# Kernel optimization log

Hardware: AMD Instinct MI355X
Metric: run time of the kernel (lower is better)

## Reference

```python
import jax, jax.numpy as jnp
import numpy as np

T, B = 2048, 32
LIS, SPE, ATT = 1024, 1024, 512


def setup_inputs() -> dict:
    key = jax.random.key(0)
    ks = jax.random.split(key, 10)
    s = 0.02
    return {
        "listener_state": jax.random.normal(ks[0], (T, B, LIS), jnp.float32),
        "speller_state": jax.random.normal(ks[1], (B, SPE), jnp.float32),
        "listener_len": jax.random.randint(ks[2], (B,), 1, T + 1),
        "batch_size": B,
        "W_score": jax.random.normal(ks[3], (LIS, ATT), jnp.float32) * s,
        "b_score": jnp.zeros((ATT,), jnp.float32),
        "W_value": jax.random.normal(ks[4], (LIS, ATT), jnp.float32) * s,
        "b_value": jnp.zeros((ATT,), jnp.float32),
        "W_proj": jax.random.normal(ks[5], (SPE, ATT), jnp.float32) * s,
        "b_proj": jnp.zeros((ATT,), jnp.float32),
    }


def reference(listener_state, speller_state, listener_len, batch_size,
              W_score, b_score, W_value, b_value, W_proj, b_proj):
    # batch_first=False path: [T,B,D] -> [B,T,D]
    x = jnp.transpose(listener_state, (1, 0, 2))
    keys = jax.nn.relu(x @ W_score + b_score)          # [B,T,A]
    vals = jax.nn.relu(x @ W_value + b_value)          # [B,T,A]
    query = jax.nn.relu(speller_state @ W_proj + b_proj)  # [B,A]
    scores = jnp.einsum('ba,bta->bt', query, keys)     # [B,T]
    # vectorized length mask: additive -100 past valid length (faithful to source)
    t = jnp.arange(keys.shape[1])
    mask = jnp.where(t[None, :] >= listener_len[:, None], -100.0, 0.0)
    attn = jax.nn.softmax(scores + mask, axis=1)       # [B,T]
    context = jnp.einsum('bt,bta->ba', attn, vals)     # [B,A]
    return (context, attn)
```

## Files before the change

kernel.cpp:

```cpp
#include <hip/hip_runtime.h>
#include <hip/hip_bf16.h>
#include <hip/hip_fp16.h>

#define T_DIM 2048
#define B_DIM 32
#define LIS_DIM 1024
#define SPE_DIM 1024
#define ATT_DIM 512

typedef _Float16 f16x8 __attribute__((ext_vector_type(8)));
typedef _Float16 f16x4 __attribute__((ext_vector_type(4)));
typedef float f32x4 __attribute__((ext_vector_type(4)));

__global__ void transpose_w_kernel(const float* __restrict__ Ws,
                                   const float* __restrict__ Wv,
                                   _Float16* __restrict__ WTf) {
  __shared__ float t17[1024 * 17];
  int blk = blockIdx.x;
  int mat = blk >> 5, ct = blk & 31;
  int tid = threadIdx.x;
  const float* W = mat ? Wv : Ws;
  for (int e = tid; e < 16384; e += 256) {
    int k = e >> 4, c = e & 15;
    t17[k * 17 + c] = W[(size_t)k * ATT_DIM + ct * 16 + c];
  }
  __syncthreads();
  int wv4 = tid >> 6, lane = tid & 63, lo = lane & 15, hi = lane >> 4;
  for (int ks = wv4; ks < 32; ks += 4) {
    f16x8 h;
#pragma unroll
    for (int j = 0; j < 8; ++j)
      h[j] = (_Float16)t17[(ks * 32 + hi * 8 + j) * 17 + lo];
    ((f16x8*)WTf)[((size_t)((mat * 32 + ct) * 32 + ks)) * 64 + lane] = h;
  }
}

__global__ void query_kernel(const float* __restrict__ spe,
                             const float* __restrict__ Wp,
                             const float* __restrict__ bp,
                             float* __restrict__ q) {
  __shared__ float s[SPE_DIM];
  int b = blockIdx.x;
  for (int i = threadIdx.x; i < SPE_DIM; i += 256) s[i] = spe[(size_t)b * SPE_DIM + i];
  __syncthreads();
  for (int a = threadIdx.x; a < ATT_DIM; a += 256) {
    float acc = bp[a];
    for (int l = 0; l < SPE_DIM; ++l)
      acc = fmaf(s[l], Wp[(size_t)l * ATT_DIM + a], acc);
    q[(size_t)b * ATT_DIM + a] = fmaxf(acc, 0.f);
  }
}

__global__ __launch_bounds__(512, 2)
void dual_gemm_kernel(const float* __restrict__ x,
                      const _Float16* __restrict__ WTf,
                      const float* __restrict__ bs,
                      const float* __restrict__ bv,
                      const float* __restrict__ q,
                      float* __restrict__ scores,
                      _Float16* __restrict__ vals_p) {
  __shared__ __align__(16) char A_lds[2][16384];
  __shared__ float bk_s[ATT_DIM], bv_s[ATT_DIM], q_s[ATT_DIM];
  __shared__ float red_s[64];

  const int tid = threadIdx.x;
  const int blk = blockIdx.x;
  const int b = blk & 31;
  const int tc = blk >> 5;
  const int t0 = tc * 64;

  bk_s[tid] = bs[tid];
  bv_s[tid] = bv[tid];
  q_s[tid] = q[(size_t)b * ATT_DIM + tid];
  if (tid < 64) red_s[tid] = 0.f;

  const float* xb = x + (size_t)b * LIS_DIM;
  const int wv = tid >> 6;
  const int lane = tid & 63;
  const int lo = lane & 15;
  const int hi = lane >> 4;

  f32x4 sl[4];
  auto stage_load = [&](int c) {
    const int k0 = c * 128;
#pragma unroll
    for (int it = 0; it < 4; ++it) {
      int idx = it * 512 + tid;
      int row = idx >> 5;
      int c4 = idx & 31;
      sl[it] = __builtin_nontemporal_load(
          (const f32x4*)(xb + (size_t)(t0 + row) * (B_DIM * LIS_DIM) + k0) + c4);
    }
  };
  auto stage_write = [&](int c) {
    char* buf = A_lds[c & 1];
#pragma unroll
    for (int it = 0; it < 4; ++it) {
      int idx = it * 512 + tid;
      int row = idx >> 5;
      int c4 = idx & 31;
      f16x4 h;
      h[0] = (_Float16)sl[it][0]; h[1] = (_Float16)sl[it][1];
      h[2] = (_Float16)sl[it][2]; h[3] = (_Float16)sl[it][3];
      int off = (row * 256 + c4 * 8) ^ ((row & 7) << 4);
      *(f16x4*)(buf + off) = h;
    }
  };

  f32x4 kacc[4][4], vacc[4][4];
#pragma unroll
  for (int m = 0; m < 4; ++m)
#pragma unroll
    for (int n = 0; n < 4; ++n) {
      kacc[m][n] = (f32x4){0.f, 0.f, 0.f, 0.f};
      vacc[m][n] = (f32x4){0.f, 0.f, 0.f, 0.f};
    }

  stage_load(0);
  stage_write(0);
  __syncthreads();

  const f16x8* Wf = (const f16x8*)WTf;
  f16x8 wkf[2][4], wvf[2][4];
#pragma unroll
  for (int n = 0; n < 4; ++n) {
    wkf[0][n] = Wf[(size_t)((wv * 4 + n) * 32 + 0) * 64 + lane];
    wvf[0][n] = Wf[(size_t)((32 + wv * 4 + n) * 32 + 0) * 64 + lane];
  }

  for (int c = 0; c < 8; ++c) {
    if (c < 7) stage_load(c + 1);
    const char* buf = A_lds[c & 1];
#pragma unroll
    for (int kki = 0; kki < 4; ++kki) {
      const int ks = c * 4 + kki;
      const int kp = (ks + 1 < 32) ? ks + 1 : 31;
      const int cur = kki & 1, nxt = cur ^ 1;
#pragma unroll
      for (int n = 0; n < 4; ++n) {
        wkf[nxt][n] = Wf[(size_t)((wv * 4 + n) * 32 + kp) * 64 + lane];
        wvf[nxt][n] = Wf[(size_t)((32 + wv * 4 + n) * 32 + kp) * 64 + lane];
      }
      f16x8 bx[4];
#pragma unroll
      for (int m = 0; m < 4; ++m) {
        int row = m * 16 + lo;
        int off = (row * 256 + kki * 64 + hi * 16) ^ ((row & 7) << 4);
        bx[m] = *(const f16x8*)(buf + off);
      }
#pragma unroll
      for (int n = 0; n < 4; ++n)
#pragma unroll
        for (int m = 0; m < 4; ++m) {
          kacc[m][n] = __builtin_amdgcn_mfma_f32_16x16x32_f16(wkf[cur][n], bx[m], kacc[m][n], 0, 0, 0);
          vacc[m][n] = __builtin_amdgcn_mfma_f32_16x16x32_f16(wvf[cur][n], bx[m], vacc[m][n], 0, 0, 0);
        }
    }
    if (c < 7) stage_write(c + 1);
    __syncthreads();
  }

  _Float16* vp = vals_p + ((size_t)(b * 32 + tc) * 8 + wv) * 4096;
#pragma unroll
  for (int m = 0; m < 4; ++m)
#pragma unroll
    for (int n = 0; n < 4; ++n) {
      int col = wv * 64 + n * 16 + hi * 4;
      f16x4 h;
#pragma unroll
      for (int r = 0; r < 4; ++r)
        h[r] = (_Float16)fmaxf(vacc[m][n][r] + bv_s[col + r], 0.f);
      __builtin_nontemporal_store(h, (f16x4*)(vp + (m * 4 + n) * 256 + lane * 4));
    }

  float sr[4] = {0.f, 0.f, 0.f, 0.f};
#pragma unroll
  for (int m = 0; m < 4; ++m)
#pragma unroll
    for (int n = 0; n < 4; ++n) {
      int col = wv * 64 + n * 16 + hi * 4;
#pragma unroll
      for (int r = 0; r < 4; ++r)
        sr[m] += q_s[col + r] * fmaxf(kacc[m][n][r] + bk_s[col + r], 0.f);
    }
#pragma unroll
  for (int m = 0; m < 4; ++m) {
    sr[m] += __shfl_xor(sr[m], 16, 64);
    sr[m] += __shfl_xor(sr[m], 32, 64);
    if (lane < 16) atomicAdd(&red_s[m * 16 + lo], sr[m]);
  }
  __syncthreads();
  if (tid < 64) scores[(size_t)b * T_DIM + t0 + tid] = red_s[tid];
}

__global__ void softmax_kernel(const float* __restrict__ scores,
                               const int* __restrict__ llen,
                               float* __restrict__ attn_out,
                               float* __restrict__ ctx_out) {
  __shared__ float rmax[4], rsum[4];
  int b = blockIdx.x, tid = threadIdx.x;
  int L = llen[b];
  float v[8];
  float mx = -1e30f;
  for (int i = 0; i < 8; ++i) {
    int t = i * 256 + tid;
    float s = scores[(size_t)b * T_DIM + t];
    if (t >= L) s -= 100.f;
    v[i] = s;
    mx = fmaxf(mx, s);
  }
  for (int d = 1; d < 64; d <<= 1) mx = fmaxf(mx, __shfl_xor(mx, d, 64));
  if ((tid & 63) == 0) rmax[tid >> 6] = mx;
  __syncthreads();
  mx = fmaxf(fmaxf(rmax[0], rmax[1]), fmaxf(rmax[2], rmax[3]));
  float sum = 0.f;
  for (int i = 0; i < 8; ++i) { v[i] = expf(v[i] - mx); sum += v[i]; }
  for (int d = 1; d < 64; d <<= 1) sum += __shfl_xor(sum, d, 64);
  if ((tid & 63) == 0) rsum[tid >> 6] = sum;
  __syncthreads();
  sum = rsum[0] + rsum[1] + rsum[2] + rsum[3];
  float inv = 1.f / sum;
  for (int i = 0; i < 8; ++i) {
    int t = i * 256 + tid;
    attn_out[(size_t)b * T_DIM + t] = v[i] * inv;
  }
  for (int i = tid; i < ATT_DIM; i += 256) ctx_out[(size_t)b * ATT_DIM + i] = 0.f;
}

__global__ __launch_bounds__(512)
void ctx_kernel(const _Float16* __restrict__ vals_p,
                const float* __restrict__ attn,
                float* __restrict__ ctx) {
  __shared__ float attn_s[256];
  int blk = blockIdx.x;
  int b = blk >> 3, tcg = blk & 7;
  int tid = threadIdx.x;
  int wv = tid >> 6, lane = tid & 63, lo = lane & 15, hi = lane >> 4;
  if (tid < 256) attn_s[tid] = attn[(size_t)b * T_DIM + tcg * 256 + tid];
  __syncthreads();
  float cacc[4][4] = {};
  for (int i = 0; i < 4; ++i) {
    int tc = tcg * 4 + i;
    const _Float16* vp = vals_p + ((size_t)(b * 32 + tc) * 8 + wv) * 4096;
#pragma unroll
    for (int m = 0; m < 4; ++m) {
      float w = attn_s[i * 64 + m * 16 + lo];
#pragma unroll
      for (int n = 0; n < 4; ++n) {
        f16x4 v = __builtin_nontemporal_load(
            (const f16x4*)(vp + (m * 4 + n) * 256 + lane * 4));
#pragma unroll
        for (int r = 0; r < 4; ++r) cacc[n][r] += w * (float)v[r];
      }
    }
  }
#pragma unroll
  for (int n = 0; n < 4; ++n)
#pragma unroll
    for (int r = 0; r < 4; ++r) {
      float v = cacc[n][r];
      v += __shfl_xor(v, 1, 64);
      v += __shfl_xor(v, 2, 64);
      v += __shfl_xor(v, 4, 64);
      v += __shfl_xor(v, 8, 64);
      if (lo == 0)
        atomicAdd(&ctx[(size_t)b * ATT_DIM + wv * 64 + n * 16 + hi * 4 + r], v);
    }
}

extern "C" void kernel_launch(void* const* d_in, const int* in_sizes, int n_in,
                              void* d_out, int out_size, void* d_ws, size_t ws_size,
                              hipStream_t stream) {
  const float* x   = (const float*)d_in[0];
  const float* spe = (const float*)d_in[1];
  const int*   len = (const int*)d_in[2];
  const float* Ws  = (const float*)d_in[4];
  const float* bs  = (const float*)d_in[5];
  const float* Wv  = (const float*)d_in[6];
  const float* bv  = (const float*)d_in[7];
  const float* Wp  = (const float*)d_in[8];
  const float* bp  = (const float*)d_in[9];
  float* out = (float*)d_out;

  char* ws = (char*)d_ws;
  _Float16* WTf  = (_Float16*)ws;
  float* q       = (float*)(ws + (2u << 20));
  float* scores  = (float*)(ws + (2u << 20) + (64u << 10));
  _Float16* vals = (_Float16*)(ws + (4u << 20));

  transpose_w_kernel<<<dim3(64), dim3(256), 0, stream>>>(Ws, Wv, WTf);
  query_kernel<<<dim3(32), dim3(256), 0, stream>>>(spe, Wp, bp, q);
  dual_gemm_kernel<<<dim3(1024), dim3(512), 0, stream>>>(x, WTf, bs, bv, q, scores, vals);
  softmax_kernel<<<dim3(32), dim3(256), 0, stream>>>(scores, len, out + 16384, out);
  ctx_kernel<<<dim3(256), dim3(512), 0, stream>>>(vals, out + 16384, out);
}
```

Before: 253.9 us.

## Fuse softmax-weighted context into dual GEMM with flash-style partial reductions

Each dual GEMM block now applies the length mask, computes a local max and exp-sum over its 64 timesteps, and reduces exp-weighted ReLU values into a per-block partial context vector. This removes the fp16 vals intermediate (written and then re-read through global memory) and replaces the separate softmax and context kernels with one small final kernel. That kernel rescales the partials by exp(local max minus global max) and also writes the attention weights. The cost is extra epilogue work and shuffle reductions in the GEMM kernel, plus a small fp32 partial buffer.

New measurement: 257.9 us. About the same (+1.6%).

```diff
diff --git a/kernel.cpp b/kernel.cpp
--- a/kernel.cpp
+++ b/kernel.cpp
@@ -57,17 +57,22 @@
                       const float* __restrict__ bs,
                       const float* __restrict__ bv,
                       const float* __restrict__ q,
+                      const int* __restrict__ llen,
                       float* __restrict__ scores,
-                      _Float16* __restrict__ vals_p) {
+                      float* __restrict__ partM,
+                      float* __restrict__ partZ,
+                      float* __restrict__ Npart) {
   __shared__ __align__(16) char A_lds[2][16384];
   __shared__ float bk_s[ATT_DIM], bv_s[ATT_DIM], q_s[ATT_DIM];
   __shared__ float red_s[64];
+  __shared__ float pb_s[64];
 
   const int tid = threadIdx.x;
   const int blk = blockIdx.x;
   const int b = blk & 31;
   const int tc = blk >> 5;
   const int t0 = tc * 64;
+  const int L = llen[b];
 
   bk_s[tid] = bs[tid];
   bv_s[tid] = bv[tid];
@@ -160,19 +165,6 @@
     __syncthreads();
   }
 
-  _Float16* vp = vals_p + ((size_t)(b * 32 + tc) * 8 + wv) * 4096;
-#pragma unroll
-  for (int m = 0; m < 4; ++m)
-#pragma unroll
-    for (int n = 0; n < 4; ++n) {
-      int col = wv * 64 + n * 16 + hi * 4;
-      f16x4 h;
-#pragma unroll
-      for (int r = 0; r < 4; ++r)
-        h[r] = (_Float16)fmaxf(vacc[m][n][r] + bv_s[col + r], 0.f);
-      __builtin_nontemporal_store(h, (f16x4*)(vp + (m * 4 + n) * 256 + lane * 4));
-    }
-
   float sr[4] = {0.f, 0.f, 0.f, 0.f};
 #pragma unroll
   for (int m = 0; m < 4; ++m)
@@ -190,82 +182,92 @@
     if (lane < 16) atomicAdd(&red_s[m * 16 + lo], sr[m]);
   }
   __syncthreads();
-  if (tid < 64) scores[(size_t)b * T_DIM + t0 + tid] = red_s[tid];
-}
-
-__global__ void softmax_kernel(const float* __restrict__ scores,
-                               const int* __restrict__ llen,
-                               float* __restrict__ attn_out,
-                               float* __restrict__ ctx_out) {
-  __shared__ float rmax[4], rsum[4];
+
+  if (wv == 0) {
+    float s = red_s[lane] + ((t0 + lane) >= L ? -100.f : 0.f);
+    scores[(size_t)b * T_DIM + t0 + lane] = s;
+    float mx = s;
+#pragma unroll
+    for (int d = 1; d < 64; d <<= 1) mx = fmaxf(mx, __shfl_xor(mx, d, 64));
+    float p = expf(s - mx);
+    float z = p;
+#pragma unroll
+    for (int d = 1; d < 64; d <<= 1) z += __shfl_xor(z, d, 64);
+    pb_s[lane] = p;
+    if (lane == 0) {
+      partM[b * 32 + tc] = mx;
+      partZ[b * 32 + tc] = z;
+    }
+  }
+  __syncthreads();
+
+  float cs[4][4] = {};
+#pragma unroll
+  for (int m = 0; m < 4; ++m) {
+    float p = pb_s[m * 16 + lo];
+#pragma unroll
+    for (int n = 0; n < 4; ++n) {
+      int col = wv * 64 + n * 16 + hi * 4;
+#pragma unroll
+      for (int r = 0; r < 4; ++r)
+        cs[n][r] += p * fmaxf(vacc[m][n][r] + bv_s[col + r], 0.f);
+    }
+  }
+#pragma unroll
+  for (int n = 0; n < 4; ++n)
+#pragma unroll
+    for (int r = 0; r < 4; ++r) {
+      cs[n][r] += __shfl_xor(cs[n][r], 1, 64);
+      cs[n][r] += __shfl_xor(cs[n][r], 2, 64);
+      cs[n][r] += __shfl_xor(cs[n][r], 4, 64);
+      cs[n][r] += __shfl_xor(cs[n][r], 8, 64);
+    }
+  if (lo == 0) {
+    float* Np = Npart + ((size_t)(b * 32 + tc)) * ATT_DIM;
+#pragma unroll
+    for (int n = 0; n < 4; ++n) {
+      f32x4 v = {cs[n][0], cs[n][1], cs[n][2], cs[n][3]};
+      *(f32x4*)(Np + wv * 64 + n * 16 + hi * 4) = v;
+    }
+  }
+}
+
+__global__ __launch_bounds__(512)
+void final_kernel(const float* __restrict__ scores,
+                  const float* __restrict__ partM,
+                  const float* __restrict__ partZ,
+                  const float* __restrict__ Npart,
+                  float* __restrict__ ctx_out,
+                  float* __restrict__ attn_out) {
+  __shared__ float sc_s[32];
+  __shared__ float MZ[2];
   int b = blockIdx.x, tid = threadIdx.x;
-  int L = llen[b];
-  float v[8];
-  float mx = -1e30f;
-  for (int i = 0; i < 8; ++i) {
-    int t = i * 256 + tid;
-    float s = scores[(size_t)b * T_DIM + t];
-    if (t >= L) s -= 100.f;
-    v[i] = s;
-    mx = fmaxf(mx, s);
-  }
-  for (int d = 1; d < 64; d <<= 1) mx = fmaxf(mx, __shfl_xor(mx, d, 64));
-  if ((tid & 63) == 0) rmax[tid >> 6] = mx;
-  __syncthreads();
-  mx = fmaxf(fmaxf(rmax[0], rmax[1]), fmaxf(rmax[2], rmax[3]));
-  float sum = 0.f;
-  for (int i = 0; i < 8; ++i) { v[i] = expf(v[i] - mx); sum += v[i]; }
-  for (int d = 1; d < 64; d <<= 1) sum += __shfl_xor(sum, d, 64);
-  if ((tid & 63) == 0) rsum[tid >> 6] = sum;
-  __syncthreads();
-  sum = rsum[0] + rsum[1] + rsum[2] + rsum[3];
-  float inv = 1.f / sum;
-  for (int i = 0; i < 8; ++i) {
-    int t = i * 256 + tid;
-    attn_out[(size_t)b * T_DIM + t] = v[i] * inv;
-  }
-  for (int i = tid; i < ATT_DIM; i += 256) ctx_out[(size_t)b * ATT_DIM + i] = 0.f;
-}
-
-__global__ __launch_bounds__(512)
-void ctx_kernel(const _Float16* __restrict__ vals_p,
-                const float* __restrict__ attn,
-                float* __restrict__ ctx) {
-  __shared__ float attn_s[256];
-  int blk = blockIdx.x;
-  int b = blk >> 3, tcg = blk & 7;
-  int tid = threadIdx.x;
-  int wv = tid >> 6, lane = tid & 63, lo = lane & 15, hi = lane >> 4;
-  if (tid < 256) attn_s[tid] = attn[(size_t)b * T_DIM + tcg * 256 + tid];
-  __syncthreads();
-  float cacc[4][4] = {};
+  int lane = tid & 63;
+  if (tid < 64) {
+    float pm = (lane < 32) ? partM[b * 32 + lane] : -1e30f;
+    float mx = pm;
+#pragma unroll
+    for (int d = 1; d < 64; d <<= 1) mx = fmaxf(mx, __shfl_xor(mx, d, 64));
+    float e = (lane < 32) ? expf(pm - mx) : 0.f;
+    float z = ((lane < 32) ? partZ[b * 32 + lane] : 0.f) * e;
+#pragma unroll
+    for (int d = 1; d < 64; d <<= 1) z += __shfl_xor(z, d, 64);
+    if (lane < 32) sc_s[lane] = e;
+    if (lane == 0) { MZ[0] = mx; MZ[1] = 1.f / z; }
+  }
+  __syncthreads();
+  const float M = MZ[0], invZ = MZ[1];
+#pragma unroll
   for (int i = 0; i < 4; ++i) {
-    int tc = tcg * 4 + i;
-    const _Float16* vp = vals_p + ((size_t)(b * 32 + tc) * 8 + wv) * 4096;
-#pragma unroll
-    for (int m = 0; m < 4; ++m) {
-      float w = attn_s[i * 64 + m * 16 + lo];
-#pragma unroll
-      for (int n = 0; n < 4; ++n) {
-        f16x4 v = __builtin_nontemporal_load(
-            (const f16x4*)(vp + (m * 4 + n) * 256 + lane * 4));
-#pragma unroll
-        for (int r = 0; r < 4; ++r) cacc[n][r] += w * (float)v[r];
-      }
-    }
-  }
-#pragma unroll
-  for (int n = 0; n < 4; ++n)
-#pragma unroll
-    for (int r = 0; r < 4; ++r) {
-      float v = cacc[n][r];
-      v += __shfl_xor(v, 1, 64);
-      v += __shfl_xor(v, 2, 64);
-      v += __shfl_xor(v, 4, 64);
-      v += __shfl_xor(v, 8, 64);
-      if (lo == 0)
-        atomicAdd(&ctx[(size_t)b * ATT_DIM + wv * 64 + n * 16 + hi * 4 + r], v);
-    }
+    int t = i * 512 + tid;
+    attn_out[(size_t)b * T_DIM + t] = expf(scores[(size_t)b * T_DIM + t] - M) * invZ;
+  }
+  float acc = 0.f;
+  const float* Np = Npart + (size_t)b * 32 * ATT_DIM;
+#pragma unroll 8
+  for (int tcc = 0; tcc < 32; ++tcc)
+    acc = fmaf(sc_s[tcc], Np[tcc * ATT_DIM + tid], acc);
+  ctx_out[(size_t)b * ATT_DIM + tid] = acc * invZ;
 }
 
 extern "C" void kernel_launch(void* const* d_in, const int* in_sizes, int n_in,
@@ -283,14 +285,17 @@
   float* out = (float*)d_out;
 
   char* ws = (char*)d_ws;
-  _Float16* WTf  = (_Float16*)ws;
-  float* q       = (float*)(ws + (2u << 20));
-  float* scores  = (float*)(ws + (2u << 20) + (64u << 10));
-  _Float16* vals = (_Float16*)(ws + (4u << 20));
+  _Float16* WTf = (_Float16*)ws;
+  float* q      = (float*)(ws + (2u << 20));
+  float* scores = (float*)(ws + (2u << 20) + (64u << 10));
+  float* partM  = (float*)(ws + (2u << 20) + (320u << 10));
+  float* partZ  = (float*)(ws + (2u << 20) + (324u << 10));
+  float* Npart  = (float*)(ws + (2u << 20) + (328u << 10));
 
   transpose_w_kernel<<<dim3(64), dim3(256), 0, stream>>>(Ws, Wv, WTf);
   query_kernel<<<dim3(32), dim3(256), 0, stream>>>(spe, Wp, bp, q);
-  dual_gemm_kernel<<<dim3(1024), dim3(512), 0, stream>>>(x, WTf, bs, bv, q, scores, vals);
-  softmax_kernel<<<dim3(32), dim3(256), 0, stream>>>(scores, len, out + 16384, out);
-  ctx_kernel<<<dim3(256), dim3(512), 0, stream>>>(vals, out + 16384, out);
-}
+  dual_gemm_kernel<<<dim3(1024), dim3(512), 0, stream>>>(
+      x, WTf, bs, bv, q, len, scores, partM, partZ, Npart);
+  final_kernel<<<dim3(32), dim3(512), 0, stream>>>(
+      scores, partM, partZ, Npart, out, out + 16384);
+}
```

## Split dual GEMM by weight matrix with 128-row tiles; merge prep kernels

Applied to the files above, without the earlier changes.

Each GEMM block now computes only one of the key or value projections over a 128-row time tile instead of both over 64 rows, and the block count stays the same. The aim is to halve the per-block weight fragment loads and the accumulator register pressure per matrix. The cost is that every x tile is now read and converted twice, once for keys and once for values. The weight transpose and the query projection are merged into one launch to save a kernel launch, and the vals layout and ctx kernel indexing are updated to the 128-row tiles.

After: 341.7 us. 34.6% more time.

```diff
diff --git a/kernel.cpp b/kernel.cpp
--- a/kernel.cpp
+++ b/kernel.cpp
@@ -12,67 +12,68 @@
 typedef _Float16 f16x4 __attribute__((ext_vector_type(4)));
 typedef float f32x4 __attribute__((ext_vector_type(4)));
 
-__global__ void transpose_w_kernel(const float* __restrict__ Ws,
-                                   const float* __restrict__ Wv,
-                                   _Float16* __restrict__ WTf) {
-  __shared__ float t17[1024 * 17];
+__global__ void prep_kernel(const float* __restrict__ Ws,
+                            const float* __restrict__ Wv,
+                            _Float16* __restrict__ WTf,
+                            const float* __restrict__ spe,
+                            const float* __restrict__ Wp,
+                            const float* __restrict__ bp,
+                            float* __restrict__ q) {
   int blk = blockIdx.x;
-  int mat = blk >> 5, ct = blk & 31;
   int tid = threadIdx.x;
-  const float* W = mat ? Wv : Ws;
-  for (int e = tid; e < 16384; e += 256) {
-    int k = e >> 4, c = e & 15;
-    t17[k * 17 + c] = W[(size_t)k * ATT_DIM + ct * 16 + c];
-  }
-  __syncthreads();
-  int wv4 = tid >> 6, lane = tid & 63, lo = lane & 15, hi = lane >> 4;
-  for (int ks = wv4; ks < 32; ks += 4) {
-    f16x8 h;
-#pragma unroll
-    for (int j = 0; j < 8; ++j)
-      h[j] = (_Float16)t17[(ks * 32 + hi * 8 + j) * 17 + lo];
-    ((f16x8*)WTf)[((size_t)((mat * 32 + ct) * 32 + ks)) * 64 + lane] = h;
-  }
-}
-
-__global__ void query_kernel(const float* __restrict__ spe,
-                             const float* __restrict__ Wp,
-                             const float* __restrict__ bp,
-                             float* __restrict__ q) {
-  __shared__ float s[SPE_DIM];
-  int b = blockIdx.x;
-  for (int i = threadIdx.x; i < SPE_DIM; i += 256) s[i] = spe[(size_t)b * SPE_DIM + i];
-  __syncthreads();
-  for (int a = threadIdx.x; a < ATT_DIM; a += 256) {
-    float acc = bp[a];
-    for (int l = 0; l < SPE_DIM; ++l)
-      acc = fmaf(s[l], Wp[(size_t)l * ATT_DIM + a], acc);
-    q[(size_t)b * ATT_DIM + a] = fmaxf(acc, 0.f);
+  if (blk < 64) {
+    __shared__ float t17[1024 * 17];
+    int mat = blk >> 5, ct = blk & 31;
+    const float* W = mat ? Wv : Ws;
+    for (int e = tid; e < 16384; e += 256) {
+      int k = e >> 4, c = e & 15;
+      t17[k * 17 + c] = W[(size_t)k * ATT_DIM + ct * 16 + c];
+    }
+    __syncthreads();
+    int wv4 = tid >> 6, lane = tid & 63, lo = lane & 15, hi = lane >> 4;
+    for (int ks = wv4; ks < 32; ks += 4) {
+      f16x8 h;
+#pragma unroll
+      for (int j = 0; j < 8; ++j)
+        h[j] = (_Float16)t17[(ks * 32 + hi * 8 + j) * 17 + lo];
+      ((f16x8*)WTf)[((size_t)((mat * 32 + ct) * 32 + ks)) * 64 + lane] = h;
+    }
+  } else {
+    __shared__ float s[SPE_DIM];
+    int b = blk - 64;
+    for (int i = tid; i < SPE_DIM; i += 256) s[i] = spe[(size_t)b * SPE_DIM + i];
+    __syncthreads();
+    for (int a = tid; a < ATT_DIM; a += 256) {
+      float acc = bp[a];
+      for (int l = 0; l < SPE_DIM; ++l)
+        acc = fmaf(s[l], Wp[(size_t)l * ATT_DIM + a], acc);
+      q[(size_t)b * ATT_DIM + a] = fmaxf(acc, 0.f);
+    }
   }
 }
 
 __global__ __launch_bounds__(512, 2)
-void dual_gemm_kernel(const float* __restrict__ x,
-                      const _Float16* __restrict__ WTf,
-                      const float* __restrict__ bs,
-                      const float* __restrict__ bv,
-                      const float* __restrict__ q,
-                      float* __restrict__ scores,
-                      _Float16* __restrict__ vals_p) {
-  __shared__ __align__(16) char A_lds[2][16384];
-  __shared__ float bk_s[ATT_DIM], bv_s[ATT_DIM], q_s[ATT_DIM];
-  __shared__ float red_s[64];
+void gemm_split_kernel(const float* __restrict__ x,
+                       const _Float16* __restrict__ WTf,
+                       const float* __restrict__ bs,
+                       const float* __restrict__ bv,
+                       const float* __restrict__ q,
+                       float* __restrict__ scores,
+                       _Float16* __restrict__ vals_p) {
+  __shared__ __align__(16) char A_lds[2][32768];
+  __shared__ float bias_s[ATT_DIM], q_s[ATT_DIM];
+  __shared__ float red_s[128];
 
   const int tid = threadIdx.x;
   const int blk = blockIdx.x;
-  const int b = blk & 31;
-  const int tc = blk >> 5;
-  const int t0 = tc * 64;
-
-  bk_s[tid] = bs[tid];
-  bv_s[tid] = bv[tid];
+  const int mat = blk & 1;
+  const int b   = (blk >> 1) & 31;
+  const int tc  = blk >> 6;
+  const int t0  = tc * 128;
+
+  bias_s[tid] = mat ? bv[tid] : bs[tid];
   q_s[tid] = q[(size_t)b * ATT_DIM + tid];
-  if (tid < 64) red_s[tid] = 0.f;
+  if (tid < 128) red_s[tid] = 0.f;
 
   const float* xb = x + (size_t)b * LIS_DIM;
   const int wv = tid >> 6;
@@ -80,11 +81,11 @@
   const int lo = lane & 15;
   const int hi = lane >> 4;
 
-  f32x4 sl[4];
+  f32x4 sl[8];
   auto stage_load = [&](int c) {
     const int k0 = c * 128;
 #pragma unroll
-    for (int it = 0; it < 4; ++it) {
+    for (int it = 0; it < 8; ++it) {
       int idx = it * 512 + tid;
       int row = idx >> 5;
       int c4 = idx & 31;
@@ -95,7 +96,7 @@
   auto stage_write = [&](int c) {
     char* buf = A_lds[c & 1];
 #pragma unroll
-    for (int it = 0; it < 4; ++it) {
+    for (int it = 0; it < 8; ++it) {
       int idx = it * 512 + tid;
       int row = idx >> 5;
       int c4 = idx & 31;
@@ -107,26 +108,22 @@
     }
   };
 
-  f32x4 kacc[4][4], vacc[4][4];
-#pragma unroll
-  for (int m = 0; m < 4; ++m)
-#pragma unroll
-    for (int n = 0; n < 4; ++n) {
-      kacc[m][n] = (f32x4){0.f, 0.f, 0.f, 0.f};
-      vacc[m][n] = (f32x4){0.f, 0.f, 0.f, 0.f};
-    }
+  f32x4 acc[8][4];
+#pragma unroll
+  for (int m = 0; m < 8; ++m)
+#pragma unroll
+    for (int n = 0; n < 4; ++n)
+      acc[m][n] = (f32x4){0.f, 0.f, 0.f, 0.f};
 
   stage_load(0);
   stage_write(0);
   __syncthreads();
 
   const f16x8* Wf = (const f16x8*)WTf;
-  f16x8 wkf[2][4], wvf[2][4];
-#pragma unroll
-  for (int n = 0; n < 4; ++n) {
-    wkf[0][n] = Wf[(size_t)((wv * 4 + n) * 32 + 0) * 64 + lane];
-    wvf[0][n] = Wf[(size_t)((32 + wv * 4 + n) * 32 + 0) * 64 + lane];
-  }
+  f16x8 wf[2][4];
+#pragma unroll
+  for (int n = 0; n < 4; ++n)
+    wf[0][n] = Wf[(size_t)((mat * 32 + wv * 4 + n) * 32 + 0) * 64 + lane];
 
   for (int c = 0; c < 8; ++c) {
     if (c < 7) stage_load(c + 1);
@@ -137,13 +134,11 @@
       const int kp = (ks + 1 < 32) ? ks + 1 : 31;
       const int cur = kki & 1, nxt = cur ^ 1;
 #pragma unroll
-      for (int n = 0; n < 4; ++n) {
-        wkf[nxt][n] = Wf[(size_t)((wv * 4 + n) * 32 + kp) * 64 + lane];
-        wvf[nxt][n] = Wf[(size_t)((32 + wv * 4 + n) * 32 + kp) * 64 + lane];
-      }
-      f16x8 bx[4];
-#pragma unroll
-      for (int m = 0; m < 4; ++m) {
+      for (int n = 0; n < 4; ++n)
+        wf[nxt][n] = Wf[(size_t)((mat * 32 + wv * 4 + n) * 32 + kp) * 64 + lane];
+      f16x8 bx[8];
+#pragma unroll
+      for (int m = 0; m < 8; ++m) {
         int row = m * 16 + lo;
         int off = (row * 256 + kki * 64 + hi * 16) ^ ((row & 7) << 4);
         bx[m] = *(const f16x8*)(buf + off);
@@ -151,46 +146,48 @@
 #pragma unroll
       for (int n = 0; n < 4; ++n)
 #pragma unroll
-        for (int m = 0; m < 4; ++m) {
-          kacc[m][n] = __builtin_amdgcn_mfma_f32_16x16x32_f16(wkf[cur][n], bx[m], kacc[m][n], 0, 0, 0);
-          vacc[m][n] = __builtin_amdgcn_mfma_f32_16x16x32_f16(wvf[cur][n], bx[m], vacc[m][n], 0, 0, 0);
-        }
+        for (int m = 0; m < 8; ++m)
+          acc[m][n] = __builtin_amdgcn_mfma_f32_16x16x32_f16(wf[cur][n], bx[m], acc[m][n], 0, 0, 0);
     }
     if (c < 7) stage_write(c + 1);
     __syncthreads();
   }
 
-  _Float16* vp = vals_p + ((size_t)(b * 32 + tc) * 8 + wv) * 4096;
-#pragma unroll
-  for (int m = 0; m < 4; ++m)
-#pragma unroll
-    for (int n = 0; n < 4; ++n) {
-      int col = wv * 64 + n * 16 + hi * 4;
-      f16x4 h;
-#pragma unroll
-      for (int r = 0; r < 4; ++r)
-        h[r] = (_Float16)fmaxf(vacc[m][n][r] + bv_s[col + r], 0.f);
-      __builtin_nontemporal_store(h, (f16x4*)(vp + (m * 4 + n) * 256 + lane * 4));
-    }
-
-  float sr[4] = {0.f, 0.f, 0.f, 0.f};
-#pragma unroll
-  for (int m = 0; m < 4; ++m)
-#pragma unroll
-    for (int n = 0; n < 4; ++n) {
-      int col = wv * 64 + n * 16 + hi * 4;
-#pragma unroll
-      for (int r = 0; r < 4; ++r)
-        sr[m] += q_s[col + r] * fmaxf(kacc[m][n][r] + bk_s[col + r], 0.f);
-    }
-#pragma unroll
-  for (int m = 0; m < 4; ++m) {
-    sr[m] += __shfl_xor(sr[m], 16, 64);
-    sr[m] += __shfl_xor(sr[m], 32, 64);
-    if (lane < 16) atomicAdd(&red_s[m * 16 + lo], sr[m]);
-  }
-  __syncthreads();
-  if (tid < 64) scores[(size_t)b * T_DIM + t0 + tid] = red_s[tid];
+  if (mat == 0) {
+    float sr[8];
+#pragma unroll
+    for (int m = 0; m < 8; ++m) sr[m] = 0.f;
+#pragma unroll
+    for (int m = 0; m < 8; ++m)
+#pragma unroll
+      for (int n = 0; n < 4; ++n) {
+        int col = wv * 64 + n * 16 + hi * 4;
+#pragma unroll
+        for (int r = 0; r < 4; ++r)
+          sr[m] += q_s[col + r] * fmaxf(acc[m][n][r] + bias_s[col + r], 0.f);
+      }
+#pragma unroll
+    for (int m = 0; m < 8; ++m) {
+      sr[m] += __shfl_xor(sr[m], 16, 64);
+      sr[m] += __shfl_xor(sr[m], 32, 64);
+      if (lane < 16) atomicAdd(&red_s[m * 16 + lo], sr[m]);
+    }
+    __syncthreads();
+    if (tid < 128) scores[(size_t)b * T_DIM + t0 + tid] = red_s[tid];
+  } else {
+    _Float16* vp = vals_p + ((size_t)(b * 16 + tc) * 8 + wv) * 8192;
+#pragma unroll
+    for (int m = 0; m < 8; ++m)
+#pragma unroll
+      for (int n = 0; n < 4; ++n) {
+        int col = wv * 64 + n * 16 + hi * 4;
+        f16x4 h;
+#pragma unroll
+        for (int r = 0; r < 4; ++r)
+          h[r] = (_Float16)fmaxf(acc[m][n][r] + bias_s[col + r], 0.f);
+        __builtin_nontemporal_store(h, (f16x4*)(vp + (m * 4 + n) * 256 + lane * 4));
+      }
+  }
 }
 
 __global__ void softmax_kernel(const float* __restrict__ scores,
@@ -233,18 +230,18 @@
                 float* __restrict__ ctx) {
   __shared__ float attn_s[256];
   int blk = blockIdx.x;
-  int b = blk >> 3, tcg = blk & 7;
+  int b = blk >> 3, tg = blk & 7;
   int tid = threadIdx.x;
   int wv = tid >> 6, lane = tid & 63, lo = lane & 15, hi = lane >> 4;
-  if (tid < 256) attn_s[tid] = attn[(size_t)b * T_DIM + tcg * 256 + tid];
+  if (tid < 256) attn_s[tid] = attn[(size_t)b * T_DIM + tg * 256 + tid];
   __syncthreads();
   float cacc[4][4] = {};
-  for (int i = 0; i < 4; ++i) {
-    int tc = tcg * 4 + i;
-    const _Float16* vp = vals_p + ((size_t)(b * 32 + tc) * 8 + wv) * 4096;
-#pragma unroll
-    for (int m = 0; m < 4; ++m) {
-      float w = attn_s[i * 64 + m * 16 + lo];
+  for (int i = 0; i < 2; ++i) {
+    int tc = tg * 2 + i;
+    const _Float16* vp = vals_p + ((size_t)(b * 16 + tc) * 8 + wv) * 8192;
+#pragma unroll
+    for (int m = 0; m < 8; ++m) {
+      float w = attn_s[i * 128 + m * 16 + lo];
 #pragma unroll
       for (int n = 0; n < 4; ++n) {
         f16x4 v = __builtin_nontemporal_load(
@@ -288,9 +285,9 @@
   float* scores  = (float*)(ws + (2u << 20) + (64u << 10));
   _Float16* vals = (_Float16*)(ws + (4u << 20));
 
-  transpose_w_kernel<<<dim3(64), dim3(256), 0, stream>>>(Ws, Wv, WTf);
-  query_kernel<<<dim3(32), dim3(256), 0, stream>>>(spe, Wp, bp, q);
-  dual_gemm_kernel<<<dim3(1024), dim3(512), 0, stream>>>(x, WTf, bs, bv, q, scores, vals);
+  prep_kernel<<<dim3(96), dim3(256), 0, stream>>>(Ws, Wv, WTf, spe, Wp, bp, q);
+  gemm_split_kernel<<<dim3(1024), dim3(512), 0, stream>>>(
+      x, WTf, bs, bv, q, scores, vals);
   softmax_kernel<<<dim3(32), dim3(256), 0, stream>>>(scores, len, out + 16384, out);
   ctx_kernel<<<dim3(256), dim3(512), 0, stream>>>(vals, out + 16384, out);
 }
```

## Interleave global prefetch with MFMA steps and merge prep kernels

Applied to the files above, without the earlier changes.

Spreads the next-chunk global loads across the four k-substeps, one slice per substep, instead of issuing them all at once. Each MFMA block is wrapped with explicit barriers, an lgkmcnt wait, a sched_barrier and setprio raised around the MFMAs, so waves stay in lockstep and give priority to matrix work. It also fuses the weight-transpose and query kernels into one launch to save launch overhead. The extra per-substep barriers can add synchronisation stalls.

New measurement: 365.4 us. +43.9%, slower.

```diff
diff --git a/kernel.cpp b/kernel.cpp
--- a/kernel.cpp
+++ b/kernel.cpp
@@ -12,42 +12,43 @@
 typedef _Float16 f16x4 __attribute__((ext_vector_type(4)));
 typedef float f32x4 __attribute__((ext_vector_type(4)));
 
-__global__ void transpose_w_kernel(const float* __restrict__ Ws,
-                                   const float* __restrict__ Wv,
-                                   _Float16* __restrict__ WTf) {
-  __shared__ float t17[1024 * 17];
+__global__ void prep_kernel(const float* __restrict__ Ws,
+                            const float* __restrict__ Wv,
+                            _Float16* __restrict__ WTf,
+                            const float* __restrict__ spe,
+                            const float* __restrict__ Wp,
+                            const float* __restrict__ bp,
+                            float* __restrict__ q) {
   int blk = blockIdx.x;
-  int mat = blk >> 5, ct = blk & 31;
   int tid = threadIdx.x;
-  const float* W = mat ? Wv : Ws;
-  for (int e = tid; e < 16384; e += 256) {
-    int k = e >> 4, c = e & 15;
-    t17[k * 17 + c] = W[(size_t)k * ATT_DIM + ct * 16 + c];
-  }
-  __syncthreads();
-  int wv4 = tid >> 6, lane = tid & 63, lo = lane & 15, hi = lane >> 4;
-  for (int ks = wv4; ks < 32; ks += 4) {
-    f16x8 h;
-#pragma unroll
-    for (int j = 0; j < 8; ++j)
-      h[j] = (_Float16)t17[(ks * 32 + hi * 8 + j) * 17 + lo];
-    ((f16x8*)WTf)[((size_t)((mat * 32 + ct) * 32 + ks)) * 64 + lane] = h;
-  }
-}
-
-__global__ void query_kernel(const float* __restrict__ spe,
-                             const float* __restrict__ Wp,
-                             const float* __restrict__ bp,
-                             float* __restrict__ q) {
-  __shared__ float s[SPE_DIM];
-  int b = blockIdx.x;
-  for (int i = threadIdx.x; i < SPE_DIM; i += 256) s[i] = spe[(size_t)b * SPE_DIM + i];
-  __syncthreads();
-  for (int a = threadIdx.x; a < ATT_DIM; a += 256) {
-    float acc = bp[a];
-    for (int l = 0; l < SPE_DIM; ++l)
-      acc = fmaf(s[l], Wp[(size_t)l * ATT_DIM + a], acc);
-    q[(size_t)b * ATT_DIM + a] = fmaxf(acc, 0.f);
+  if (blk < 64) {
+    __shared__ float t17[1024 * 17];
+    int mat = blk >> 5, ct = blk & 31;
+    const float* W = mat ? Wv : Ws;
+    for (int e = tid; e < 16384; e += 256) {
+      int k = e >> 4, c = e & 15;
+      t17[k * 17 + c] = W[(size_t)k * ATT_DIM + ct * 16 + c];
+    }
+    __syncthreads();
+    int wv4 = tid >> 6, lane = tid & 63, lo = lane & 15, hi = lane >> 4;
+    for (int ks = wv4; ks < 32; ks += 4) {
+      f16x8 h;
+#pragma unroll
+      for (int j = 0; j < 8; ++j)
+        h[j] = (_Float16)t17[(ks * 32 + hi * 8 + j) * 17 + lo];
+      ((f16x8*)WTf)[((size_t)((mat * 32 + ct) * 32 + ks)) * 64 + lane] = h;
+    }
+  } else {
+    __shared__ float s[SPE_DIM];
+    int b = blk - 64;
+    for (int i = tid; i < SPE_DIM; i += 256) s[i] = spe[(size_t)b * SPE_DIM + i];
+    __syncthreads();
+    for (int a = tid; a < ATT_DIM; a += 256) {
+      float acc = bp[a];
+      for (int l = 0; l < SPE_DIM; ++l)
+        acc = fmaf(s[l], Wp[(size_t)l * ATT_DIM + a], acc);
+      q[(size_t)b * ATT_DIM + a] = fmaxf(acc, 0.f);
+    }
   }
 }
 
@@ -81,16 +82,13 @@
   const int hi = lane >> 4;
 
   f32x4 sl[4];
-  auto stage_load = [&](int c) {
+  auto stage_load_one = [&](int c, int it) {
     const int k0 = c * 128;
-#pragma unroll
-    for (int it = 0; it < 4; ++it) {
-      int idx = it * 512 + tid;
-      int row = idx >> 5;
-      int c4 = idx & 31;
-      sl[it] = __builtin_nontemporal_load(
-          (const f32x4*)(xb + (size_t)(t0 + row) * (B_DIM * LIS_DIM) + k0) + c4);
-    }
+    int idx = it * 512 + tid;
+    int row = idx >> 5;
+    int c4 = idx & 31;
+    sl[it] = __builtin_nontemporal_load(
+        (const f32x4*)(xb + (size_t)(t0 + row) * (B_DIM * LIS_DIM) + k0) + c4);
   };
   auto stage_write = [&](int c) {
     char* buf = A_lds[c & 1];
@@ -116,9 +114,11 @@
       vacc[m][n] = (f32x4){0.f, 0.f, 0.f, 0.f};
     }
 
-  stage_load(0);
+#pragma unroll
+  for (int it = 0; it < 4; ++it) stage_load_one(0, it);
   stage_write(0);
-  __syncthreads();
+  asm volatile("s_waitcnt lgkmcnt(0)" ::: "memory");
+  __builtin_amdgcn_s_barrier();
 
   const f16x8* Wf = (const f16x8*)WTf;
   f16x8 wkf[2][4], wvf[2][4];
@@ -129,7 +129,6 @@
   }
 
   for (int c = 0; c < 8; ++c) {
-    if (c < 7) stage_load(c + 1);
     const char* buf = A_lds[c & 1];
 #pragma unroll
     for (int kki = 0; kki < 4; ++kki) {
@@ -141,6 +140,7 @@
         wkf[nxt][n] = Wf[(size_t)((wv * 4 + n) * 32 + kp) * 64 + lane];
         wvf[nxt][n] = Wf[(size_t)((32 + wv * 4 + n) * 32 + kp) * 64 + lane];
       }
+      if (c < 7) stage_load_one(c + 1, kki);
       f16x8 bx[4];
 #pragma unroll
       for (int m = 0; m < 4; ++m) {
@@ -148,6 +148,10 @@
         int off = (row * 256 + kki * 64 + hi * 16) ^ ((row & 7) << 4);
         bx[m] = *(const f16x8*)(buf + off);
       }
+      __builtin_amdgcn_s_barrier();
+      asm volatile("s_waitcnt lgkmcnt(0)" ::: "memory");
+      __builtin_amdgcn_sched_barrier(0);
+      __builtin_amdgcn_s_setprio(1);
 #pragma unroll
       for (int n = 0; n < 4; ++n)
 #pragma unroll
@@ -155,9 +159,14 @@
           kacc[m][n] = __builtin_amdgcn_mfma_f32_16x16x32_f16(wkf[cur][n], bx[m], kacc[m][n], 0, 0, 0);
           vacc[m][n] = __builtin_amdgcn_mfma_f32_16x16x32_f16(wvf[cur][n], bx[m], vacc[m][n], 0, 0, 0);
         }
-    }
-    if (c < 7) stage_write(c + 1);
-    __syncthreads();
+      __builtin_amdgcn_s_setprio(0);
+      __builtin_amdgcn_s_barrier();
+    }
+    if (c < 7) {
+      stage_write(c + 1);
+      asm volatile("s_waitcnt lgkmcnt(0)" ::: "memory");
+      __builtin_amdgcn_s_barrier();
+    }
   }
 
   _Float16* vp = vals_p + ((size_t)(b * 32 + tc) * 8 + wv) * 4096;
@@ -288,9 +297,9 @@
   float* scores  = (float*)(ws + (2u << 20) + (64u << 10));
   _Float16* vals = (_Float16*)(ws + (4u << 20));
 
-  transpose_w_kernel<<<dim3(64), dim3(256), 0, stream>>>(Ws, Wv, WTf);
-  query_kernel<<<dim3(32), dim3(256), 0, stream>>>(spe, Wp, bp, q);
-  dual_gemm_kernel<<<dim3(1024), dim3(512), 0, stream>>>(x, WTf, bs, bv, q, scores, vals);
+  prep_kernel<<<dim3(96), dim3(256), 0, stream>>>(Ws, Wv, WTf, spe, Wp, bp, q);
+  dual_gemm_kernel<<<dim3(1024), dim3(512), 0, stream>>>(
+      x, WTf, bs, bv, q, scores, vals);
   softmax_kernel<<<dim3(32), dim3(256), 0, stream>>>(scores, len, out + 16384, out);
   ctx_kernel<<<dim3(256), dim3(512), 0, stream>>>(vals, out + 16384, out);
 }
```
